# Performance work log

Measured on AMD Instinct MI355X. Metric: run time of the kernel, lower is better.

Reference implementation:

```python
import jax, jax.numpy as jnp
import numpy as np

B, D, E = 4096, 768, 8
L = (32 // E) * D  # per-expert latents = 3072
K = 32             # topk


def setup_inputs() -> dict:
    key = jax.random.key(0)
    ks = jax.random.split(key, 8)
    x = jax.random.normal(ks[0], (B, D), dtype=jnp.float32)
    router_w = jax.random.normal(ks[1], (E, D), dtype=jnp.float32) / np.sqrt(D)
    router_b = jnp.zeros((E,), dtype=jnp.float32)
    W_enc = jax.random.normal(ks[2], (E, L, D), dtype=jnp.float32) / np.sqrt(D)
    b_enc = jnp.zeros((E, L), dtype=jnp.float32)
    W_dec = jax.random.normal(ks[3], (E, L, D), dtype=jnp.float32)
    # normalize_decoder=True: unit-norm decoder rows
    W_dec = W_dec / jnp.linalg.norm(W_dec, axis=-1, keepdims=True)
    b_dec = jnp.zeros((E, D), dtype=jnp.float32)
    return {"x": x, "router_w": router_w, "router_b": router_b,
            "W_enc": W_enc, "b_enc": b_enc, "W_dec": W_dec, "b_dec": b_dec}


def reference(x, router_w, router_b, W_enc, b_enc, W_dec, b_dec):
    Bx = x.shape[0]
    # --- router (top-1) ---
    logits = x @ router_w.T + router_b            # [B, E]
    expert_ids = jnp.argmax(logits, axis=-1)      # [B]
    probs = jax.nn.softmax(logits, axis=-1)
    sel_probs = jnp.max(probs, axis=-1)           # prob of argmax expert

    # --- load-balance loss ---
    counts = jnp.zeros((E,), jnp.float32).at[expert_ids].add(1.0)
    freq = counts / Bx
    load_balance_loss = jnp.sum((freq - 1.0 / E) ** 2)

    sae_out = jnp.zeros_like(x)
    latent_acts = jnp.zeros((Bx, K), x.dtype)
    latent_indices = jnp.zeros((Bx, K), jnp.int32)
    total_fvu = jnp.float32(0.0)
    rows = jnp.arange(Bx)[:, None]

    for e in range(E):  # fixed small expert loop
        mask = expert_ids == e                    # [B]
        mf = mask.astype(x.dtype)[:, None]        # [B,1]
        n = jnp.sum(mf)
        # encode: TopK SAE, pre-acts on (x - b_dec)
        pre = jax.nn.relu((x - b_dec[e]) @ W_enc[e].T + b_enc[e])   # [B, L]
        acts, idx = jax.lax.top_k(pre, K)                            # [B, K]
        # decode via dense sparse-latent matmul
        z = jnp.zeros((Bx, L), x.dtype).at[rows, idx].set(acts)      # [B, L]
        recon = z @ W_dec[e] + b_dec[e]                              # [B, D]
        # combine: weight by router prob, scatter by mask
        sae_out = sae_out + mf * recon * sel_probs[:, None]
        latent_acts = jnp.where(mask[:, None], acts, latent_acts)
        latent_indices = jnp.where(mask[:, None], idx, latent_indices)
        # per-expert FVU over its tokens (unweighted reconstruction)
        mean_e = jnp.sum(x * mf, axis=0) / jnp.maximum(n, 1.0)
        var_e = jnp.sum(mf * (x - mean_e) ** 2)
        l2_e = jnp.sum(mf * (x - recon) ** 2)
        fvu_e = jnp.where((n > 0) & (var_e > 0), l2_e / jnp.maximum(var_e, 1e-12), 0.0)
        total_fvu = total_fvu + fvu_e * n

    fvu = total_fvu / Bx
    auxk_loss = jnp.float32(0.0)       # dead_mask=None
    multi_topk_fvu = jnp.float32(0.0)  # multi_topk=False
    return (sae_out, latent_acts, latent_indices, fvu, auxk_loss,
            multi_topk_fvu, expert_ids, load_balance_loss)
```

## Files before the change

kernel.cpp:

```cpp
#include <hip/hip_runtime.h>
#include <math.h>

#define B_TOK 4096
#define D_DIM 768
#define E_NUM 8
#define L_LAT 3072
#define K_TOP 32

#define O_SAE  0
#define O_ACTS (B_TOK*D_DIM)
#define O_IDX  (O_ACTS + B_TOK*K_TOP)
#define O_FVU  (O_IDX + B_TOK*K_TOP)
#define O_AUX  (O_FVU + 1)
#define O_MTK  (O_AUX + 1)
#define O_EID  (O_MTK + 1)
#define O_LBL  (O_EID + B_TOK)

struct Ws {
  double S[E_NUM][D_DIM];
  double S2[E_NUM][D_DIM];
  double var_[E_NUM];
  double l2[E_NUM];
  float  sel[B_TOK];
  int    eid[B_TOK];
  int    perm[B_TOK];
  int    counts[E_NUM];
  int    off[E_NUM + 1];
  int    ytab_e[48];
  int    ytab_y[48];
  int    nslots;
  int    pad[15];
};

__global__ void init_k(Ws* ws, float* out) {
  int tid = threadIdx.x;
  if (tid < E_NUM) { ws->counts[tid] = 0; ws->l2[tid] = 0.0; }
  if (tid == 0) { out[O_AUX] = 0.0f; out[O_MTK] = 0.0f; }
}

__global__ void router_k(const float* __restrict__ x, const float* __restrict__ rw,
                         const float* __restrict__ rb, Ws* ws, float* out) {
  int t = blockIdx.x;
  int lane = threadIdx.x;
  double acc[E_NUM];
#pragma unroll
  for (int e = 0; e < E_NUM; ++e) acc[e] = 0.0;
  const float* xr = x + (size_t)t * D_DIM;
#pragma unroll
  for (int j = 0; j < D_DIM / 64; ++j) {
    int d = lane + 64 * j;
    float xv = xr[d];
#pragma unroll
    for (int e = 0; e < E_NUM; ++e) acc[e] += (double)xv * (double)rw[e * D_DIM + d];
  }
#pragma unroll
  for (int e = 0; e < E_NUM; ++e) {
#pragma unroll
    for (int o = 32; o; o >>= 1) acc[e] += __shfl_down(acc[e], o);
  }
  if (lane == 0) {
    double lg[E_NUM];
    int be = 0; double bm = -1e300;
#pragma unroll
    for (int e = 0; e < E_NUM; ++e) {
      lg[e] = acc[e] + (double)rb[e];
      if (lg[e] > bm) { bm = lg[e]; be = e; }
    }
    double s = 0.0;
#pragma unroll
    for (int e = 0; e < E_NUM; ++e) s += exp(lg[e] - bm);
    ws->sel[t] = (float)(1.0 / s);
    ws->eid[t] = be;
    atomicAdd(&ws->counts[be], 1);
    out[O_EID + t] = (float)be;
  }
}

__global__ void scan_k(Ws* ws, float* out) {
  if (threadIdx.x == 0) {
    int o = 0; double loss = 0.0;
    int slot = 0;
    for (int e = 0; e < E_NUM; ++e) {
      ws->off[e] = o;
      int c = ws->counts[e];
      o += c;
      double f = (double)c / (double)B_TOK - 1.0 / (double)E_NUM;
      loss += f * f;
      int nb = (c + 127) / 128;
      for (int b = 0; b < nb; ++b) { ws->ytab_e[slot] = e; ws->ytab_y[slot] = b; ++slot; }
    }
    ws->off[E_NUM] = o;
    ws->nslots = slot;
    out[O_LBL] = (float)loss;
  }
}

__global__ void group_k(Ws* ws) {
  int e = blockIdx.x, tid = threadIdx.x;
  __shared__ int cnt[256];
  const int CH = B_TOK / 256;
  int i0 = tid * CH;
  int c = 0;
#pragma unroll
  for (int i = 0; i < CH; ++i) c += (ws->eid[i0 + i] == e) ? 1 : 0;
  cnt[tid] = c;
  __syncthreads();
  int excl = 0;
  for (int i = 0; i < tid; ++i) excl += cnt[i];
  int base = ws->off[e] + excl;
  for (int i = 0; i < CH; ++i) {
    int t = i0 + i;
    if (ws->eid[t] == e) ws->perm[base++] = t;
  }
}

__global__ void stats_k(const float* __restrict__ x, Ws* ws) {
  int e = blockIdx.x, dg = blockIdx.y;
  int tid = threadIdx.x;
  int dl = tid & 31, strip = tid >> 5;
  int d = dg * 32 + dl;
  int s0 = ws->off[e], s1 = ws->off[e + 1];
  double S = 0.0, S2 = 0.0;
  for (int i = s0 + strip; i < s1; i += 8) {
    float xv = x[(size_t)ws->perm[i] * D_DIM + d];
    S += (double)xv;
    S2 += (double)xv * (double)xv;
  }
  __shared__ double sS[256], sS2[256];
  sS[tid] = S; sS2[tid] = S2;
  __syncthreads();
  for (int s = 128; s >= 32; s >>= 1) {
    if (tid < s) { sS[tid] += sS[tid + s]; sS2[tid] += sS2[tid + s]; }
    __syncthreads();
  }
  if (tid < 32) { ws->S[e][d] = sS[tid]; ws->S2[e][d] = sS2[tid]; }
}

__global__ void var_k(Ws* ws) {
  int e = blockIdx.x, tid = threadIdx.x;
  int n = ws->counts[e];
  double nd = (double)((n > 0) ? n : 1);
  double acc = 0.0;
  for (int d = tid; d < D_DIM; d += 256) {
    double S = ws->S[e][d], S2 = ws->S2[e][d];
    double m = S / nd;
    acc += S2 - 2.0 * m * S + (double)n * m * m;
  }
  __shared__ double red[256];
  red[tid] = acc;
  __syncthreads();
  for (int s = 128; s; s >>= 1) {
    if (tid < s) red[tid] += red[tid + s];
    __syncthreads();
  }
  if (tid == 0) ws->var_[e] = red[0];
}

#define KTILE(ACC, K0) do {                                                    \
  __syncthreads();                                                             \
  _Pragma("unroll")                                                            \
  for (int p = 0; p < 4; ++p) {                                                \
    int idx = p * 256 + tid;                                                   \
    int r = idx >> 3, c4 = (idx & 7) * 4;                                      \
    float4 xv = *(const float4*)(x + (size_t)tokrow[r] * D_DIM + (K0) + c4);   \
    float4 bv = *(const float4*)(bdec + e * D_DIM + (K0) + c4);                \
    float4 xm = make_float4(xv.x - bv.x, xv.y - bv.y, xv.z - bv.z, xv.w - bv.w);\
    *(float4*)&xs[r][c4] = xm;                                                 \
    *(float4*)&wsh[r][c4] =                                                    \
        *(const float4*)(We + wb + (size_t)(bl + r) * D_DIM + (K0) + c4);      \
  }                                                                            \
  __syncthreads();                                                             \
  _Pragma("unroll")                                                            \
  for (int q = 0; q < 8; ++q) {                                                \
    float4 a[8];                                                               \
    _Pragma("unroll")                                                          \
    for (int i = 0; i < 8; ++i) a[i] = *(const float4*)&xs[ty + 16 * i][q * 4];\
    _Pragma("unroll")                                                          \
    for (int j = 0; j < 8; ++j) {                                              \
      float4 b = *(const float4*)&wsh[tx + 16 * j][q * 4];                     \
      _Pragma("unroll")                                                        \
      for (int i = 0; i < 8; ++i) {                                            \
        ACC[i][j] = fmaf(a[i].x, b.x, ACC[i][j]);                              \
        ACC[i][j] = fmaf(a[i].y, b.y, ACC[i][j]);                              \
        ACC[i][j] = fmaf(a[i].z, b.z, ACC[i][j]);                              \
        ACC[i][j] = fmaf(a[i].w, b.w, ACC[i][j]);                              \
      }                                                                        \
    }                                                                          \
  }                                                                            \
} while (0)

__launch_bounds__(256, 2)
__global__ void gemm_k(const float* __restrict__ x, const float* __restrict__ We,
                       const float* __restrict__ benc, const float* __restrict__ bdec,
                       Ws* ws, float* __restrict__ pre) {
  int slot = blockIdx.y;
  if (slot >= ws->nslots) return;
  int e = ws->ytab_e[slot];
  int bt = ws->ytab_y[slot] * 128;
  int n0 = ws->off[e], n1 = ws->off[e + 1];
  int ne = n1 - n0;
  int bl = blockIdx.x * 128;

  __shared__ float xs[128][36];
  __shared__ float wsh[128][36];
  __shared__ int tokrow[128];

  int tid = threadIdx.x;
  if (tid < 128) {
    int srow = bt + tid;
    tokrow[tid] = ws->perm[n0 + (srow < ne ? srow : 0)];
  }

  int tx = tid & 15, ty = tid >> 4;
  size_t wb = (size_t)e * L_LAT * D_DIM;

  float acc[8][8] = {{0.f}};

  for (int k0 = 0; k0 < 512; k0 += 32) KTILE(acc, k0);
#pragma unroll
  for (int i = 0; i < 8; ++i) {
    int srow = bt + ty + 16 * i;
    if (srow < ne) {
      float* pr = &pre[(size_t)(n0 + srow) * L_LAT + bl];
#pragma unroll
      for (int j = 0; j < 8; ++j) pr[tx + 16 * j] = acc[i][j];
    }
  }

#pragma unroll
  for (int i = 0; i < 8; ++i)
#pragma unroll
    for (int j = 0; j < 8; ++j) acc[i][j] = 0.f;
  for (int k0 = 512; k0 < 768; k0 += 32) KTILE(acc, k0);

#pragma unroll
  for (int i = 0; i < 8; ++i) {
    int srow = bt + ty + 16 * i;
    if (srow < ne) {
      float* pr = &pre[(size_t)(n0 + srow) * L_LAT + bl];
#pragma unroll
      for (int j = 0; j < 8; ++j) {
        int lc = tx + 16 * j;
        float r = (pr[lc] + acc[i][j]) + benc[e * L_LAT + bl + lc];
        pr[lc] = fmaxf(r, 0.0f);
      }
    }
  }
}

__launch_bounds__(256)
__global__ void topk_k(const float* __restrict__ pre, Ws* ws, float* out) {
  __shared__ float buf[4][L_LAT];
  int tid = threadIdx.x, wave = tid >> 6, lane = tid & 63;
  int s = blockIdx.x * 4 + wave;
  int t = ws->perm[s];
  const float* src = pre + (size_t)s * L_LAT;

  unsigned long long bk = 0ULL;
#pragma unroll
  for (int j = 0; j < L_LAT / 256; ++j) {
    int l = lane * 4 + 256 * j;
    float4 v = *(const float4*)(src + l);
    *(float4*)&buf[wave][l] = v;
    const float* vp = &v.x;
#pragma unroll
    for (int c = 0; c < 4; ++c) {
      unsigned long long key = ((unsigned long long)__float_as_uint(vp[c]) << 32)
                             | (unsigned long long)(0xFFFFFFFFu - (unsigned)(l + c));
      if (key > bk) bk = key;
    }
  }

  for (int k = 0; k < K_TOP; ++k) {
    unsigned long long m = bk;
#pragma unroll
    for (int o = 32; o; o >>= 1) {
      unsigned long long o2 = __shfl_down(m, o);
      if (o2 > m) m = o2;
    }
    m = __shfl(m, 0);
    int l = (int)(0xFFFFFFFFu - (unsigned)(m & 0xFFFFFFFFull));
    float v = __uint_as_float((unsigned)(m >> 32));
    if (lane == 0) {
      out[O_ACTS + (size_t)t * K_TOP + k] = v;
      out[O_IDX + (size_t)t * K_TOP + k] = (float)l;
    }
    if (((l >> 2) & 63) == lane) {
      buf[wave][l] = -1.0f;
      bk = 0ULL;
#pragma unroll
      for (int j = 0; j < L_LAT / 256; ++j) {
        int ll = lane * 4 + 256 * j;
        float4 vv = *(const float4*)&buf[wave][ll];
        const float* vp = &vv.x;
#pragma unroll
        for (int c = 0; c < 4; ++c) {
          if (vp[c] >= 0.0f) {
            unsigned long long key = ((unsigned long long)__float_as_uint(vp[c]) << 32)
                                   | (unsigned long long)(0xFFFFFFFFu - (unsigned)(ll + c));
            if (key > bk) bk = key;
          }
        }
      }
    }
  }
}

__launch_bounds__(192)
__global__ void decode_k(const float* __restrict__ x, const float* __restrict__ Wdec,
                         const float* __restrict__ bdec, Ws* ws, float* out) {
  int s = blockIdx.x, tid = threadIdx.x;
  int t = ws->perm[s];
  int e = ws->eid[t];
  float sp = ws->sel[t];
  __shared__ float sa[K_TOP];
  __shared__ int si[K_TOP];
  if (tid < K_TOP) {
    sa[tid] = out[O_ACTS + (size_t)t * K_TOP + tid];
    si[tid] = (int)out[O_IDX + (size_t)t * K_TOP + tid];
  }
  __syncthreads();
  int d4 = tid * 4;
  float4 r = make_float4(0.f, 0.f, 0.f, 0.f);
  const float* wdb = Wdec + (size_t)e * L_LAT * D_DIM;
#pragma unroll 8
  for (int k = 0; k < K_TOP; ++k) {
    float4 w = *(const float4*)(wdb + (size_t)si[k] * D_DIM + d4);
    float a = sa[k];
    r.x = fmaf(a, w.x, r.x);
    r.y = fmaf(a, w.y, r.y);
    r.z = fmaf(a, w.z, r.z);
    r.w = fmaf(a, w.w, r.w);
  }
  float4 bd = *(const float4*)(bdec + e * D_DIM + d4);
  float4 rec = make_float4(r.x + bd.x, r.y + bd.y, r.z + bd.z, r.w + bd.w);
  float4 xr = *(const float4*)(x + (size_t)t * D_DIM + d4);
  float4 so = make_float4(rec.x * sp, rec.y * sp, rec.z * sp, rec.w * sp);
  *(float4*)&out[O_SAE + (size_t)t * D_DIM + d4] = so;
  double d0 = (double)(xr.x - rec.x);
  double d1 = (double)(xr.y - rec.y);
  double d2 = (double)(xr.z - rec.z);
  double d3 = (double)(xr.w - rec.w);
  double l2p = d0 * d0 + d1 * d1 + d2 * d2 + d3 * d3;
  __shared__ double red[192];
  red[tid] = l2p;
  __syncthreads();
  for (int s2 = 96; s2 >= 3; s2 >>= 1) {
    if (tid < s2) red[tid] += red[tid + s2];
    __syncthreads();
  }
  if (tid == 0) atomicAdd(&ws->l2[e], red[0] + red[1] + red[2]);
}

__global__ void final_k(Ws* ws, float* out) {
  if (threadIdx.x == 0) {
    double tot = 0.0;
    for (int e = 0; e < E_NUM; ++e) {
      int n = ws->counts[e];
      double v = ws->var_[e];
      if (n > 0 && v > 0.0) tot += ws->l2[e] / fmax(v, 1e-12) * (double)n;
    }
    out[O_FVU] = (float)(tot / (double)B_TOK);
  }
}

extern "C" void kernel_launch(void* const* d_in, const int* in_sizes, int n_in,
                              void* d_out, int out_size, void* d_ws, size_t ws_size,
                              hipStream_t stream) {
  const float* x  = (const float*)d_in[0];
  const float* rw = (const float*)d_in[1];
  const float* rb = (const float*)d_in[2];
  const float* We = (const float*)d_in[3];
  const float* be = (const float*)d_in[4];
  const float* Wd = (const float*)d_in[5];
  const float* bd = (const float*)d_in[6];
  float* out = (float*)d_out;
  Ws* ws = (Ws*)d_ws;
  float* pre = (float*)((char*)d_ws + ((sizeof(Ws) + 255) & ~(size_t)255));

  hipLaunchKernelGGL(init_k,   dim3(1),           dim3(64),  0, stream, ws, out);
  hipLaunchKernelGGL(router_k, dim3(B_TOK),       dim3(64),  0, stream, x, rw, rb, ws, out);
  hipLaunchKernelGGL(scan_k,   dim3(1),           dim3(64),  0, stream, ws, out);
  hipLaunchKernelGGL(group_k,  dim3(E_NUM),       dim3(256), 0, stream, ws);
  hipLaunchKernelGGL(stats_k,  dim3(E_NUM, 24),   dim3(256), 0, stream, x, ws);
  hipLaunchKernelGGL(gemm_k,   dim3(24, 40),      dim3(256), 0, stream, x, We, be, bd, ws, pre);
  hipLaunchKernelGGL(var_k,    dim3(E_NUM),       dim3(256), 0, stream, ws);
  hipLaunchKernelGGL(topk_k,   dim3(B_TOK / 4),   dim3(256), 0, stream, pre, ws, out);
  hipLaunchKernelGGL(decode_k, dim3(B_TOK),       dim3(192), 0, stream, x, Wd, bd, ws, out);
  hipLaunchKernelGGL(final_k,  dim3(1),           dim3(64),  0, stream, ws, out);
}
```

Baseline: 703.9 us.

## Fuse topk with decode, merge scan into group and var into final

Fuses the top-k selection and sparse decode into one kernel in which each wave keeps its selected activations and indices in registers and computes the reconstruction, output and L2 error directly. This removes the round trip through the output buffer and the separate decode launch. The scan work is folded into group_k and the variance kernel into final_k, cutting launch count. It also changes the GEMM row mapping so each thread owns 8 contiguous rows instead of strided rows. The trade-offs are higher register pressure in the fused kernel and one wave now handling a full 768-wide decode row.

New measurement: 703.0 us. Within noise of the previous version (-0.1%).

```diff
diff --git a/kernel.cpp b/kernel.cpp
--- a/kernel.cpp
+++ b/kernel.cpp
@@ -76,28 +76,31 @@
   }
 }
 
-__global__ void scan_k(Ws* ws, float* out) {
-  if (threadIdx.x == 0) {
-    int o = 0; double loss = 0.0;
-    int slot = 0;
-    for (int e = 0; e < E_NUM; ++e) {
-      ws->off[e] = o;
-      int c = ws->counts[e];
-      o += c;
-      double f = (double)c / (double)B_TOK - 1.0 / (double)E_NUM;
-      loss += f * f;
-      int nb = (c + 127) / 128;
-      for (int b = 0; b < nb; ++b) { ws->ytab_e[slot] = e; ws->ytab_y[slot] = b; ++slot; }
-    }
-    ws->off[E_NUM] = o;
-    ws->nslots = slot;
-    out[O_LBL] = (float)loss;
-  }
-}
-
-__global__ void group_k(Ws* ws) {
+__global__ void group_k(Ws* ws, float* out) {
   int e = blockIdx.x, tid = threadIdx.x;
   __shared__ int cnt[256];
+  __shared__ int base_sh;
+  if (tid == 0) {
+    int o = 0;
+    for (int e2 = 0; e2 < e; ++e2) o += ws->counts[e2];
+    base_sh = o;
+    if (e == 0) {
+      int o2 = 0, slot = 0; double loss = 0.0;
+      for (int e2 = 0; e2 < E_NUM; ++e2) {
+        ws->off[e2] = o2;
+        int c = ws->counts[e2];
+        o2 += c;
+        double f = (double)c / (double)B_TOK - 1.0 / (double)E_NUM;
+        loss += f * f;
+        int nb = (c + 127) / 128;
+        for (int b = 0; b < nb; ++b) { ws->ytab_e[slot] = e2; ws->ytab_y[slot] = b; ++slot; }
+      }
+      ws->off[E_NUM] = o2;
+      ws->nslots = slot;
+      out[O_LBL] = (float)loss;
+    }
+  }
+  __syncthreads();
   const int CH = B_TOK / 256;
   int i0 = tid * CH;
   int c = 0;
@@ -107,7 +110,7 @@
   __syncthreads();
   int excl = 0;
   for (int i = 0; i < tid; ++i) excl += cnt[i];
-  int base = ws->off[e] + excl;
+  int base = base_sh + excl;
   for (int i = 0; i < CH; ++i) {
     int t = i0 + i;
     if (ws->eid[t] == e) ws->perm[base++] = t;
@@ -134,26 +137,6 @@
     __syncthreads();
   }
   if (tid < 32) { ws->S[e][d] = sS[tid]; ws->S2[e][d] = sS2[tid]; }
-}
-
-__global__ void var_k(Ws* ws) {
-  int e = blockIdx.x, tid = threadIdx.x;
-  int n = ws->counts[e];
-  double nd = (double)((n > 0) ? n : 1);
-  double acc = 0.0;
-  for (int d = tid; d < D_DIM; d += 256) {
-    double S = ws->S[e][d], S2 = ws->S2[e][d];
-    double m = S / nd;
-    acc += S2 - 2.0 * m * S + (double)n * m * m;
-  }
-  __shared__ double red[256];
-  red[tid] = acc;
-  __syncthreads();
-  for (int s = 128; s; s >>= 1) {
-    if (tid < s) red[tid] += red[tid + s];
-    __syncthreads();
-  }
-  if (tid == 0) ws->var_[e] = red[0];
 }
 
 #define KTILE(ACC, K0) do {                                                    \
@@ -174,7 +157,7 @@
   for (int q = 0; q < 8; ++q) {                                                \
     float4 a[8];                                                               \
     _Pragma("unroll")                                                          \
-    for (int i = 0; i < 8; ++i) a[i] = *(const float4*)&xs[ty + 16 * i][q * 4];\
+    for (int i = 0; i < 8; ++i) a[i] = *(const float4*)&xs[ty * 8 + i][q * 4]; \
     _Pragma("unroll")                                                          \
     for (int j = 0; j < 8; ++j) {                                              \
       float4 b = *(const float4*)&wsh[tx + 16 * j][q * 4];                     \
@@ -219,7 +202,7 @@
   for (int k0 = 0; k0 < 512; k0 += 32) KTILE(acc, k0);
 #pragma unroll
   for (int i = 0; i < 8; ++i) {
-    int srow = bt + ty + 16 * i;
+    int srow = bt + ty * 8 + i;
     if (srow < ne) {
       float* pr = &pre[(size_t)(n0 + srow) * L_LAT + bl];
 #pragma unroll
@@ -235,7 +218,7 @@
 
 #pragma unroll
   for (int i = 0; i < 8; ++i) {
-    int srow = bt + ty + 16 * i;
+    int srow = bt + ty * 8 + i;
     if (srow < ne) {
       float* pr = &pre[(size_t)(n0 + srow) * L_LAT + bl];
 #pragma unroll
@@ -249,11 +232,15 @@
 }
 
 __launch_bounds__(256)
-__global__ void topk_k(const float* __restrict__ pre, Ws* ws, float* out) {
+__global__ void td_k(const float* __restrict__ pre, const float* __restrict__ x,
+                     const float* __restrict__ Wdec, const float* __restrict__ bdec,
+                     Ws* ws, float* out) {
   __shared__ float buf[4][L_LAT];
   int tid = threadIdx.x, wave = tid >> 6, lane = tid & 63;
   int s = blockIdx.x * 4 + wave;
   int t = ws->perm[s];
+  int e = ws->eid[t];
+  float sp = ws->sel[t];
   const float* src = pre + (size_t)s * L_LAT;
 
   unsigned long long bk = 0ULL;
@@ -271,6 +258,8 @@
     }
   }
 
+  float av[K_TOP]; int ai[K_TOP];
+#pragma unroll 1
   for (int k = 0; k < K_TOP; ++k) {
     unsigned long long m = bk;
 #pragma unroll
@@ -281,6 +270,7 @@
     m = __shfl(m, 0);
     int l = (int)(0xFFFFFFFFu - (unsigned)(m & 0xFFFFFFFFull));
     float v = __uint_as_float((unsigned)(m >> 32));
+    av[k] = v; ai[k] = l;
     if (lane == 0) {
       out[O_ACTS + (size_t)t * K_TOP + k] = v;
       out[O_IDX + (size_t)t * K_TOP + k] = (float)l;
@@ -304,60 +294,73 @@
       }
     }
   }
-}
-
-__launch_bounds__(192)
-__global__ void decode_k(const float* __restrict__ x, const float* __restrict__ Wdec,
-                         const float* __restrict__ bdec, Ws* ws, float* out) {
-  int s = blockIdx.x, tid = threadIdx.x;
-  int t = ws->perm[s];
-  int e = ws->eid[t];
-  float sp = ws->sel[t];
-  __shared__ float sa[K_TOP];
-  __shared__ int si[K_TOP];
-  if (tid < K_TOP) {
-    sa[tid] = out[O_ACTS + (size_t)t * K_TOP + tid];
-    si[tid] = (int)out[O_IDX + (size_t)t * K_TOP + tid];
-  }
-  __syncthreads();
-  int d4 = tid * 4;
-  float4 r = make_float4(0.f, 0.f, 0.f, 0.f);
+
   const float* wdb = Wdec + (size_t)e * L_LAT * D_DIM;
+  int d0 = lane * 4;
+  float4 r0 = make_float4(0.f,0.f,0.f,0.f);
+  float4 r1 = r0, r2 = r0;
 #pragma unroll 8
   for (int k = 0; k < K_TOP; ++k) {
-    float4 w = *(const float4*)(wdb + (size_t)si[k] * D_DIM + d4);
-    float a = sa[k];
-    r.x = fmaf(a, w.x, r.x);
-    r.y = fmaf(a, w.y, r.y);
-    r.z = fmaf(a, w.z, r.z);
-    r.w = fmaf(a, w.w, r.w);
-  }
-  float4 bd = *(const float4*)(bdec + e * D_DIM + d4);
-  float4 rec = make_float4(r.x + bd.x, r.y + bd.y, r.z + bd.z, r.w + bd.w);
-  float4 xr = *(const float4*)(x + (size_t)t * D_DIM + d4);
-  float4 so = make_float4(rec.x * sp, rec.y * sp, rec.z * sp, rec.w * sp);
-  *(float4*)&out[O_SAE + (size_t)t * D_DIM + d4] = so;
-  double d0 = (double)(xr.x - rec.x);
-  double d1 = (double)(xr.y - rec.y);
-  double d2 = (double)(xr.z - rec.z);
-  double d3 = (double)(xr.w - rec.w);
-  double l2p = d0 * d0 + d1 * d1 + d2 * d2 + d3 * d3;
-  __shared__ double red[192];
-  red[tid] = l2p;
-  __syncthreads();
-  for (int s2 = 96; s2 >= 3; s2 >>= 1) {
-    if (tid < s2) red[tid] += red[tid + s2];
+    const float* wr = wdb + (size_t)ai[k] * D_DIM;
+    float a = av[k];
+    float4 w0 = *(const float4*)(wr + d0);
+    float4 w1 = *(const float4*)(wr + d0 + 256);
+    float4 w2 = *(const float4*)(wr + d0 + 512);
+    r0.x = fmaf(a, w0.x, r0.x); r0.y = fmaf(a, w0.y, r0.y);
+    r0.z = fmaf(a, w0.z, r0.z); r0.w = fmaf(a, w0.w, r0.w);
+    r1.x = fmaf(a, w1.x, r1.x); r1.y = fmaf(a, w1.y, r1.y);
+    r1.z = fmaf(a, w1.z, r1.z); r1.w = fmaf(a, w1.w, r1.w);
+    r2.x = fmaf(a, w2.x, r2.x); r2.y = fmaf(a, w2.y, r2.y);
+    r2.z = fmaf(a, w2.z, r2.z); r2.w = fmaf(a, w2.w, r2.w);
+  }
+  const float* bd = bdec + e * D_DIM;
+  const float* xr = x + (size_t)t * D_DIM;
+  float* so = out + O_SAE + (size_t)t * D_DIM;
+  double l2p = 0.0;
+#pragma unroll
+  for (int jj = 0; jj < 3; ++jj) {
+    int d = d0 + 256 * jj;
+    float4 rr = jj == 0 ? r0 : (jj == 1 ? r1 : r2);
+    float4 bv = *(const float4*)(bd + d);
+    float4 xv = *(const float4*)(xr + d);
+    float4 rec = make_float4(rr.x + bv.x, rr.y + bv.y, rr.z + bv.z, rr.w + bv.w);
+    *(float4*)(so + d) = make_float4(rec.x * sp, rec.y * sp, rec.z * sp, rec.w * sp);
+    double e0 = (double)(xv.x - rec.x), e1 = (double)(xv.y - rec.y);
+    double e2 = (double)(xv.z - rec.z), e3 = (double)(xv.w - rec.w);
+    l2p += e0 * e0 + e1 * e1 + e2 * e2 + e3 * e3;
+  }
+#pragma unroll
+  for (int o = 32; o; o >>= 1) l2p += __shfl_down(l2p, o);
+  if (lane == 0) atomicAdd(&ws->l2[e], l2p);
+}
+
+__global__ void final_k(Ws* ws, float* out) {
+  int tid = threadIdx.x;
+  __shared__ double red[256];
+  __shared__ double varr[E_NUM];
+  for (int e = 0; e < E_NUM; ++e) {
+    int n = ws->counts[e];
+    double nd = (double)((n > 0) ? n : 1);
+    double acc = 0.0;
+    for (int d = tid; d < D_DIM; d += 256) {
+      double S = ws->S[e][d], S2 = ws->S2[e][d];
+      double m = S / nd;
+      acc += S2 - 2.0 * m * S + (double)n * m * m;
+    }
+    red[tid] = acc;
     __syncthreads();
-  }
-  if (tid == 0) atomicAdd(&ws->l2[e], red[0] + red[1] + red[2]);
-}
-
-__global__ void final_k(Ws* ws, float* out) {
-  if (threadIdx.x == 0) {
+    for (int s = 128; s; s >>= 1) {
+      if (tid < s) red[tid] += red[tid + s];
+      __syncthreads();
+    }
+    if (tid == 0) varr[e] = red[0];
+    __syncthreads();
+  }
+  if (tid == 0) {
     double tot = 0.0;
     for (int e = 0; e < E_NUM; ++e) {
       int n = ws->counts[e];
-      double v = ws->var_[e];
+      double v = varr[e];
       if (n > 0 && v > 0.0) tot += ws->l2[e] / fmax(v, 1e-12) * (double)n;
     }
     out[O_FVU] = (float)(tot / (double)B_TOK);
@@ -380,12 +383,9 @@
 
   hipLaunchKernelGGL(init_k,   dim3(1),           dim3(64),  0, stream, ws, out);
   hipLaunchKernelGGL(router_k, dim3(B_TOK),       dim3(64),  0, stream, x, rw, rb, ws, out);
-  hipLaunchKernelGGL(scan_k,   dim3(1),           dim3(64),  0, stream, ws, out);
-  hipLaunchKernelGGL(group_k,  dim3(E_NUM),       dim3(256), 0, stream, ws);
+  hipLaunchKernelGGL(group_k,  dim3(E_NUM),       dim3(256), 0, stream, ws, out);
   hipLaunchKernelGGL(stats_k,  dim3(E_NUM, 24),   dim3(256), 0, stream, x, ws);
   hipLaunchKernelGGL(gemm_k,   dim3(24, 40),      dim3(256), 0, stream, x, We, be, bd, ws, pre);
-  hipLaunchKernelGGL(var_k,    dim3(E_NUM),       dim3(256), 0, stream, ws);
-  hipLaunchKernelGGL(topk_k,   dim3(B_TOK / 4),   dim3(256), 0, stream, pre, ws, out);
-  hipLaunchKernelGGL(decode_k, dim3(B_TOK),       dim3(192), 0, stream, x, Wd, bd, ws, out);
-  hipLaunchKernelGGL(final_k,  dim3(1),           dim3(64),  0, stream, ws, out);
-}
+  hipLaunchKernelGGL(td_k,     dim3(B_TOK / 4),   dim3(256), 0, stream, pre, x, Wd, bd, ws, out);
+  hipLaunchKernelGGL(final_k,  dim3(1),           dim3(256), 0, stream, ws, out);
+}
```
